# Optimization experiments

Measured on AMD Instinct MI355X. Metric: run time of the kernel, lower is better.

The kernel has to match this reference:

```python
import jax, jax.numpy as jnp
import numpy as np
import math

B, P = 64, 2048
E_DRUG, E_PATH = 512, 512
ATTN_DIM, H, DEPTH = 1024, 8, 1
HD = ATTN_DIM // (2 * H)          # head_dim = 64
SCALING = HD ** (-0.5)
LAMBDA_INIT = 0.8 - 0.6 * math.exp(-0.3 * DEPTH)
EPS_SM = 1e-20
EPS_RMS = 1e-5


def stable_softmax(x, eps=EPS_SM):
    x = x.astype(jnp.float32)
    x = x - jnp.max(x, axis=-1, keepdims=True)
    ex = jnp.exp(x)
    return ex / (jnp.sum(ex, axis=-1, keepdims=True) + eps)


def setup_inputs() -> dict:
    key = jax.random.key(0)
    ks = jax.random.split(key, 11)
    d = 2 * H * HD  # = ATTN_DIM
    return {
        "query": jax.random.normal(ks[0], (B, 1, E_DRUG), jnp.float32),
        "key": jax.random.normal(ks[1], (B, P, E_PATH), jnp.float32),
        # Linear weights stored [in, out] (transpose of torch storage; same math)
        "Wq": jax.random.normal(ks[2], (E_DRUG, d), jnp.float32) * 0.02,
        "Wk": jax.random.normal(ks[3], (E_PATH, d), jnp.float32) * 0.02,
        "Wv": jax.random.normal(ks[4], (E_PATH, d), jnp.float32) * 0.02,
        "Wo": jax.random.normal(ks[5], (d, E_DRUG), jnp.float32) * 0.02,
        "lambda_q1": jax.random.normal(ks[6], (HD,), jnp.float32) * 0.1,
        "lambda_k1": jax.random.normal(ks[7], (HD,), jnp.float32) * 0.1,
        "lambda_q2": jax.random.normal(ks[8], (HD,), jnp.float32) * 0.1,
        "lambda_k2": jax.random.normal(ks[9], (HD,), jnp.float32) * 0.1,
        "rms_weight": jnp.ones((2 * HD,), jnp.float32),
    }


def reference(query, key, Wq, Wk, Wv, Wo,
              lambda_q1, lambda_k1, lambda_q2, lambda_k2, rms_weight):
    # Q: [B,1,H,2,HD] -> [B,H,2,1,HD]; K,V: [B,P,H,2,HD] -> [B,H,2,P,HD]
    Q = (query @ Wq).reshape(B, 1, H, 2, HD).transpose(0, 2, 3, 1, 4) * SCALING
    K = (key @ Wk).reshape(B, P, H, 2, HD).transpose(0, 2, 3, 1, 4)
    V = (key @ Wv).reshape(B, P, H, 2, HD)

    # scores: [B,H,2,1,P]
    scores = jnp.einsum('bhsqd,bhskd->bhsqk', Q, K)
    scores = stable_softmax(scores)

    lam1 = jnp.exp(jnp.sum(lambda_q1 * lambda_k1))
    lam2 = jnp.exp(jnp.sum(lambda_q2 * lambda_k2))
    lam = lam1 - lam2 + LAMBDA_INIT

    diff_attn = scores[:, :, 0] - lam * scores[:, :, 1]  # [B,H,1,P]

    V_cat = V.transpose(0, 2, 1, 3, 4).reshape(B, H, P, 2 * HD)  # [B,H,P,2HD]
    out = jnp.einsum('bhqp,bhpd->bhqd', diff_attn, V_cat)        # [B,H,1,2HD]

    # RMSNorm over last dim, affine
    var = jnp.mean(out * out, axis=-1, keepdims=True)
    out = out * jax.lax.rsqrt(var + EPS_RMS) * rms_weight
    out = out * (1.0 - LAMBDA_INIT)

    out = out.transpose(0, 2, 1, 3).reshape(B, 1, 2 * H * HD)
    out = out @ Wo  # [B,1,E_DRUG]
    return out, diff_attn
```

## Files before the change

kernel.cpp:

```cpp
#include <hip/hip_runtime.h>
#include <hip/hip_bf16.h>
#include <math.h>

#define B_ 64
#define P_ 2048
#define E_ 512
#define H_ 8
#define HD_ 64
#define D_ 1024
#define NC_ 16
#define CP_ 128
#define SMEM_FUSED (131072 + 8512 + 4352)

static constexpr float SCALING_C = 0.125f;
static constexpr float LAMBDA_INIT_C = 0.35550906759096966f;

typedef float f32x4 __attribute__((ext_vector_type(4)));
typedef float f32x2 __attribute__((ext_vector_type(2)));
typedef short bf16x8 __attribute__((ext_vector_type(8)));
typedef short bf16x4 __attribute__((ext_vector_type(4)));

static __device__ __forceinline__ short f2bf(float f) {
    unsigned u = __builtin_bit_cast(unsigned, f);
    unsigned r = (u + 0x7fffu + ((u >> 16) & 1u)) >> 16;
    return (short)r;
}

__global__ __launch_bounds__(256) void k_qproj(const float* __restrict__ query,
                                               const float* __restrict__ Wq,
                                               const float* __restrict__ Wk,
                                               unsigned short* __restrict__ qkfrag) {
    int x = blockIdx.x, b = blockIdx.y, t = threadIdx.x;
    __shared__ float q[E_];
    __shared__ float qh[256];
    q[t] = query[b * E_ + t];
    q[t + 256] = query[b * E_ + t + 256];
    __syncthreads();
    {
        int j = x * 256 + t;
        const float* w = Wq + j;
        float s0 = 0.f, s1 = 0.f, s2 = 0.f, s3 = 0.f;
        #pragma unroll 4
        for (int e = 0; e < E_; e += 4) {
            s0 += q[e]     * w[(long)e * D_];
            s1 += q[e + 1] * w[(long)(e + 1) * D_];
            s2 += q[e + 2] * w[(long)(e + 2) * D_];
            s3 += q[e + 3] * w[(long)(e + 3) * D_];
        }
        qh[t] = ((s0 + s1) + (s2 + s3)) * SCALING_C;
    }
    __syncthreads();
    int hs_loc = t >> 6, l = t & 63;
    int hs = x * 4 + hs_loc;
    int e0 = l * 8;
    const float* qp = qh + hs_loc * 64;
    float acc[8];
    #pragma unroll
    for (int jj = 0; jj < 8; ++jj) {
        const f32x4* w = (const f32x4*)(Wk + (long)(e0 + jj) * D_ + hs * HD_);
        float s = 0.f;
        #pragma unroll
        for (int d4 = 0; d4 < 16; ++d4) {
            f32x4 wv = w[d4];
            s += qp[d4 * 4 + 0] * wv[0] + qp[d4 * 4 + 1] * wv[1]
               + qp[d4 * 4 + 2] * wv[2] + qp[d4 * 4 + 3] * wv[3];
        }
        acc[jj] = s;
    }
    bf16x8 v;
    #pragma unroll
    for (int jj = 0; jj < 8; ++jj) v[jj] = f2bf(acc[jj]);
    *(bf16x8*)(qkfrag + (((long)b * 16 + (l >> 2)) * 64 + (l & 3) * 16 + hs) * 8) = v;
}

__global__ __launch_bounds__(512, 2) void k_fused512(const float* __restrict__ key,
                                                     const unsigned short* __restrict__ qkfrag,
                                                     float* __restrict__ wexp,
                                                     float* __restrict__ ms, float* __restrict__ zs,
                                                     float* __restrict__ apart) {
    extern __shared__ __align__(16) char smem[];
    unsigned short* kswz = (unsigned short*)smem;
    float* scr           = (float*)(smem + 131072);
    unsigned short* wbf  = (unsigned short*)(smem + 131072 + 8512);

    int pc = blockIdx.x, b = blockIdx.y;
    int t = threadIdx.x, wv = t >> 6, l = t & 63;

    {
        int prow = wv * 16 + (l & 15);
        const float* kp = key + ((long)b * P_ + pc * CP_ + prow) * E_ + (l >> 4) * 8;
        const bf16x8* qf = (const bf16x8*)(qkfrag + (long)b * 16 * 64 * 8) + l;
        int ebase = (l >> 4) * 8;
        int xorv = ((prow & 7) << 3) ^ ((prow & 8) << 1);
        f32x4 acc = {0.f, 0.f, 0.f, 0.f};
        #pragma unroll
        for (int s = 0; s < 16; ++s) {
            f32x4 x0 = *(const f32x4*)(kp + s * 32);
            f32x4 x1 = *(const f32x4*)(kp + s * 32 + 4);
            bf16x8 a;
            a[0] = f2bf(x0[0]); a[1] = f2bf(x0[1]); a[2] = f2bf(x0[2]); a[3] = f2bf(x0[3]);
            a[4] = f2bf(x1[0]); a[5] = f2bf(x1[1]); a[6] = f2bf(x1[2]); a[7] = f2bf(x1[3]);
            *(bf16x8*)(kswz + prow * 512 + ((ebase + 32 * s) ^ xorv)) = a;
            bf16x8 bq = qf[s * 64];
            acc = __builtin_amdgcn_mfma_f32_16x16x32_bf16(a, bq, acc, 0, 0, 0);
        }
        #pragma unroll
        for (int r = 0; r < 4; ++r)
            scr[(l & 15) * 133 + wv * 16 + (l >> 4) * 4 + r] = acc[r];
    }
    __syncthreads();

    {
        int hs = t >> 5, i = t & 31;
        const float* sr = scr + hs * 133 + i * 4;
        float v0 = sr[0], v1 = sr[1], v2 = sr[2], v3 = sr[3];
        float m = fmaxf(fmaxf(v0, v1), fmaxf(v2, v3));
        #pragma unroll
        for (int o = 16; o > 0; o >>= 1) m = fmaxf(m, __shfl_xor(m, o));
        f32x4 ev;
        ev[0] = expf(v0 - m); ev[1] = expf(v1 - m); ev[2] = expf(v2 - m); ev[3] = expf(v3 - m);
        float z = ev[0] + ev[1] + ev[2] + ev[3];
        #pragma unroll
        for (int o = 16; o > 0; o >>= 1) z += __shfl_xor(z, o);
        *(f32x4*)(wexp + ((long)b * 16 + hs) * P_ + pc * CP_ + i * 4) = ev;
        bf16x4 wb;
        wb[0] = f2bf(ev[0]); wb[1] = f2bf(ev[1]); wb[2] = f2bf(ev[2]); wb[3] = f2bf(ev[3]);
        *(bf16x4*)(wbf + hs * 136 + i * 4) = wb;
        if (i == 0) {
            ms[((long)pc * B_ + b) * 16 + hs] = m;
            zs[((long)pc * B_ + b) * 16 + hs] = z;
        }
    }
    __syncthreads();

    {
        const unsigned short* wrow = wbf + (l & 15) * 136;
        long obase = ((long)pc * B_ + b) * 16 * E_;
        #pragma unroll
        for (int tile = 0; tile < 4; ++tile) {
            int e = wv * 64 + tile * 16 + (l & 15);
            f32x4 acc = {0.f, 0.f, 0.f, 0.f};
            #pragma unroll
            for (int ks = 0; ks < 4; ++ks) {
                int pbase = ks * 32 + (l >> 4) * 8;
                bf16x8 af = *(const bf16x8*)(wrow + pbase);
                bf16x8 bfv;
                int x2 = (pbase & 8) << 1;
                #pragma unroll
                for (int j = 0; j < 8; ++j) {
                    int p = pbase + j;
                    bfv[j] = (short)kswz[p * 512 + (e ^ (j << 3) ^ x2)];
                }
                acc = __builtin_amdgcn_mfma_f32_16x16x32_bf16(af, bfv, acc, 0, 0, 0);
            }
            #pragma unroll
            for (int r = 0; r < 4; ++r) {
                int hs = (l >> 4) * 4 + r;
                apart[obase + (long)hs * E_ + e] = acc[r];
            }
        }
    }
}

__global__ __launch_bounds__(256) void k_comb(const float* __restrict__ wexp,
                                              const float* __restrict__ ms, const float* __restrict__ zs,
                                              const float* __restrict__ apart,
                                              const float* __restrict__ lq1, const float* __restrict__ lk1,
                                              const float* __restrict__ lq2, const float* __restrict__ lk2,
                                              const float* __restrict__ Wv, const float* __restrict__ rmsw,
                                              float* __restrict__ out1, float* __restrict__ on) {
    int h = blockIdx.x, b = blockIdx.y, t = threadIdx.x;
    __shared__ float lam_s;
    __shared__ float mc0s[NC_], mc1s[NC_], zc0s[NC_], zc1s[NC_];
    __shared__ float c0s[NC_], c1s[NC_];
    __shared__ float attk[E_];
    __shared__ float onred[2][128];
    __shared__ float red[4];
    int hs0 = 2 * h, hs1 = 2 * h + 1;
    if (t < 64) {
        float v1 = lq1[t] * lk1[t];
        float v2 = lq2[t] * lk2[t];
        #pragma unroll
        for (int o = 32; o > 0; o >>= 1) { v1 += __shfl_xor(v1, o); v2 += __shfl_xor(v2, o); }
        if (t == 0) lam_s = expf(v1) - expf(v2) + LAMBDA_INIT_C;
    }
    if (t >= 64 && t < 64 + NC_) {
        int c = t - 64;
        mc0s[c] = ms[((long)c * B_ + b) * 16 + hs0];
        mc1s[c] = ms[((long)c * B_ + b) * 16 + hs1];
        zc0s[c] = zs[((long)c * B_ + b) * 16 + hs0];
        zc1s[c] = zs[((long)c * B_ + b) * 16 + hs1];
    }
    __syncthreads();
    float m0 = -3.0e38f, m1 = -3.0e38f;
    #pragma unroll
    for (int c = 0; c < NC_; ++c) { m0 = fmaxf(m0, mc0s[c]); m1 = fmaxf(m1, mc1s[c]); }
    float z0 = 0.f, z1 = 0.f;
    #pragma unroll
    for (int c = 0; c < NC_; ++c) {
        z0 += zc0s[c] * expf(mc0s[c] - m0);
        z1 += zc1s[c] * expf(mc1s[c] - m1);
    }
    float lam = lam_s;
    float i0 = 1.f / (z0 + 1e-20f);
    float i1 = lam / (z1 + 1e-20f);
    if (t < NC_) {
        c0s[t] = expf(mc0s[t] - m0) * i0;
        c1s[t] = expf(mc1s[t] - m1) * i1;
    }
    __syncthreads();
    const float* w0p = wexp + ((long)b * 16 + hs0) * P_;
    const float* w1p = wexp + ((long)b * 16 + hs1) * P_;
    float* dst = out1 + ((long)b * H_ + h) * P_;
    #pragma unroll
    for (int c8 = 0; c8 < 8; ++c8) {
        int p = c8 * 256 + t;
        dst[p] = w0p[p] * c0s[p >> 7] - w1p[p] * c1s[p >> 7];
    }
    #pragma unroll
    for (int k = 0; k < 2; ++k) {
        int e = k * 256 + t;
        float s = 0.f;
        #pragma unroll 8
        for (int c = 0; c < NC_; ++c) {
            s += c0s[c] * apart[(((long)c * B_ + b) * 16 + hs0) * E_ + e]
               - c1s[c] * apart[(((long)c * B_ + b) * 16 + hs1) * E_ + e];
        }
        attk[e] = s;
    }
    __syncthreads();
    int j = t & 127, half = t >> 7;
    const float* w = Wv + (long)(half * 256) * D_ + h * 128 + j;
    const float* aa = attk + half * 256;
    float s0 = 0.f, s1 = 0.f, s2 = 0.f, s3 = 0.f;
    #pragma unroll 8
    for (int e = 0; e < 256; e += 4) {
        s0 += aa[e]     * w[(long)e * D_];
        s1 += aa[e + 1] * w[(long)(e + 1) * D_];
        s2 += aa[e + 2] * w[(long)(e + 2) * D_];
        s3 += aa[e + 3] * w[(long)(e + 3) * D_];
    }
    onred[half][j] = (s0 + s1) + (s2 + s3);
    __syncthreads();
    float v = 0.f;
    if (t < 128) v = onred[0][t] + onred[1][t];
    float sq = v * v;
    int wv2 = t >> 6, ln = t & 63;
    #pragma unroll
    for (int o = 32; o > 0; o >>= 1) sq += __shfl_xor(sq, o);
    if (ln == 0) red[wv2] = sq;
    __syncthreads();
    float tot = red[0] + red[1];
    float scale = rsqrtf(tot * (1.f / 128.f) + 1e-5f) * (1.f - LAMBDA_INIT_C);
    if (t < 128) on[(long)b * D_ + h * 128 + t] = v * scale * rmsw[t];
}

__global__ __launch_bounds__(256) void k_wo(const float* __restrict__ on,
                                            const float* __restrict__ Wo,
                                            float* __restrict__ wop) {
    int kc = blockIdx.x >> 1, oc = blockIdx.x & 1, b = blockIdx.y;
    int t = threadIdx.x;
    __shared__ float sh[256];
    sh[t] = on[(long)b * D_ + kc * 256 + t];
    __syncthreads();
    int o = oc * 256 + t;
    const float* w = Wo + (long)(kc * 256) * 512 + o;
    float s0 = 0.f, s1 = 0.f, s2 = 0.f, s3 = 0.f;
    #pragma unroll 8
    for (int k = 0; k < 256; k += 4) {
        s0 += sh[k]     * w[(long)k * 512];
        s1 += sh[k + 1] * w[(long)(k + 1) * 512];
        s2 += sh[k + 2] * w[(long)(k + 2) * 512];
        s3 += sh[k + 3] * w[(long)(k + 3) * 512];
    }
    wop[((long)kc * B_ + b) * 512 + o] = (s0 + s1) + (s2 + s3);
}

__global__ __launch_bounds__(256) void k_wored(const float* __restrict__ wop,
                                               float* __restrict__ out0) {
    int b = blockIdx.x, t = threadIdx.x;
    #pragma unroll
    for (int i = 0; i < 2; ++i) {
        int o = i * 256 + t;
        float s = 0.f;
        #pragma unroll
        for (int kc = 0; kc < 4; ++kc) s += wop[((long)kc * B_ + b) * 512 + o];
        out0[(long)b * 512 + o] = s;
    }
}

extern "C" void kernel_launch(void* const* d_in, const int* in_sizes, int n_in,
                              void* d_out, int out_size, void* d_ws, size_t ws_size,
                              hipStream_t stream) {
    const float* query = (const float*)d_in[0];
    const float* key   = (const float*)d_in[1];
    const float* Wq    = (const float*)d_in[2];
    const float* Wk    = (const float*)d_in[3];
    const float* Wv    = (const float*)d_in[4];
    const float* Wo    = (const float*)d_in[5];
    const float* lq1   = (const float*)d_in[6];
    const float* lk1   = (const float*)d_in[7];
    const float* lq2   = (const float*)d_in[8];
    const float* lk2   = (const float*)d_in[9];
    const float* rmsw  = (const float*)d_in[10];

    float* out0 = (float*)d_out;
    float* out1 = out0 + B_ * E_;

    unsigned short* qkfrag = (unsigned short*)d_ws;
    float* wexp  = (float*)d_ws + 262144;
    float* apart = wexp + (long)B_ * 16 * P_;
    float* ms    = apart + (long)NC_ * B_ * 16 * E_;
    float* zs    = ms + NC_ * B_ * 16;
    float* on    = zs + NC_ * B_ * 16;
    float* wop   = on + B_ * D_;

    static int smem_set = 0;
    if (!smem_set) {
        hipFuncSetAttribute((const void*)k_fused512,
                            hipFuncAttributeMaxDynamicSharedMemorySize, SMEM_FUSED);
        smem_set = 1;
    }

    hipLaunchKernelGGL(k_qproj,    dim3(4, B_),   dim3(256), 0, stream, query, Wq, Wk, qkfrag);
    hipLaunchKernelGGL(k_fused512, dim3(NC_, B_), dim3(512), SMEM_FUSED, stream,
                       key, qkfrag, wexp, ms, zs, apart);
    hipLaunchKernelGGL(k_comb,     dim3(H_, B_),  dim3(256), 0, stream, wexp, ms, zs, apart,
                       lq1, lk1, lq2, lk2, Wv, rmsw, out1, on);
    hipLaunchKernelGGL(k_wo,       dim3(8, B_),   dim3(256), 0, stream, on, Wo, wop);
    hipLaunchKernelGGL(k_wored,    dim3(B_),      dim3(256), 0, stream, wop, out0);
}
```

Baseline: 141.1 us.

## Halve key chunk size, store partial attention outputs as bf16 in e-major layout

The fused kernel now processes 64-position chunks with 256 threads, doubling the grid to 32 chunks per batch and roughly halving LDS use per block, which lets more blocks fit on each CU. The per-chunk attention partials are written as bf16 in an [e][16] layout, so the combine kernel reads both heads of a pair with one 32-bit load. This cuts the partial-buffer traffic, but there are twice as many chunks to combine and the partials lose precision to bf16. The attribute call is now made on every launch.

```diff
diff --git a/kernel.cpp b/kernel.cpp
--- a/kernel.cpp
+++ b/kernel.cpp
@@ -8,9 +8,11 @@
 #define H_ 8
 #define HD_ 64
 #define D_ 1024
-#define NC_ 16
-#define CP_ 128
-#define SMEM_FUSED (131072 + 8512 + 4352)
+#define NC_ 32
+#define CP_ 64
+#define SCR_ 68
+#define WBF_ 72
+#define SMEM_FUSED (65536 + 4352 + 2304)
 
 static constexpr float SCALING_C = 0.125f;
 static constexpr float LAMBDA_INIT_C = 0.35550906759096966f;
@@ -24,6 +26,9 @@
     unsigned u = __builtin_bit_cast(unsigned, f);
     unsigned r = (u + 0x7fffu + ((u >> 16) & 1u)) >> 16;
     return (short)r;
+}
+static __device__ __forceinline__ float bf2f(unsigned short s) {
+    return __builtin_bit_cast(float, (unsigned)s << 16);
 }
 
 __global__ __launch_bounds__(256) void k_qproj(const float* __restrict__ query,
@@ -73,15 +78,15 @@
     *(bf16x8*)(qkfrag + (((long)b * 16 + (l >> 2)) * 64 + (l & 3) * 16 + hs) * 8) = v;
 }
 
-__global__ __launch_bounds__(512, 2) void k_fused512(const float* __restrict__ key,
+__global__ __launch_bounds__(256, 2) void k_fused256(const float* __restrict__ key,
                                                      const unsigned short* __restrict__ qkfrag,
                                                      float* __restrict__ wexp,
                                                      float* __restrict__ ms, float* __restrict__ zs,
-                                                     float* __restrict__ apart) {
+                                                     unsigned short* __restrict__ apart) {
     extern __shared__ __align__(16) char smem[];
     unsigned short* kswz = (unsigned short*)smem;
-    float* scr           = (float*)(smem + 131072);
-    unsigned short* wbf  = (unsigned short*)(smem + 131072 + 8512);
+    float* scr           = (float*)(smem + 65536);
+    unsigned short* wbf  = (unsigned short*)(smem + 65536 + 4352);
 
     int pc = blockIdx.x, b = blockIdx.y;
     int t = threadIdx.x, wv = t >> 6, l = t & 63;
@@ -106,26 +111,26 @@
         }
         #pragma unroll
         for (int r = 0; r < 4; ++r)
-            scr[(l & 15) * 133 + wv * 16 + (l >> 4) * 4 + r] = acc[r];
+            scr[(l & 15) * SCR_ + wv * 16 + (l >> 4) * 4 + r] = acc[r];
     }
     __syncthreads();
 
     {
-        int hs = t >> 5, i = t & 31;
-        const float* sr = scr + hs * 133 + i * 4;
+        int hs = t >> 4, i = t & 15;
+        const float* sr = scr + hs * SCR_ + i * 4;
         float v0 = sr[0], v1 = sr[1], v2 = sr[2], v3 = sr[3];
         float m = fmaxf(fmaxf(v0, v1), fmaxf(v2, v3));
         #pragma unroll
-        for (int o = 16; o > 0; o >>= 1) m = fmaxf(m, __shfl_xor(m, o));
+        for (int o = 8; o > 0; o >>= 1) m = fmaxf(m, __shfl_xor(m, o));
         f32x4 ev;
         ev[0] = expf(v0 - m); ev[1] = expf(v1 - m); ev[2] = expf(v2 - m); ev[3] = expf(v3 - m);
         float z = ev[0] + ev[1] + ev[2] + ev[3];
         #pragma unroll
-        for (int o = 16; o > 0; o >>= 1) z += __shfl_xor(z, o);
+        for (int o = 8; o > 0; o >>= 1) z += __shfl_xor(z, o);
         *(f32x4*)(wexp + ((long)b * 16 + hs) * P_ + pc * CP_ + i * 4) = ev;
         bf16x4 wb;
         wb[0] = f2bf(ev[0]); wb[1] = f2bf(ev[1]); wb[2] = f2bf(ev[2]); wb[3] = f2bf(ev[3]);
-        *(bf16x4*)(wbf + hs * 136 + i * 4) = wb;
+        *(bf16x4*)(wbf + hs * WBF_ + i * 4) = wb;
         if (i == 0) {
             ms[((long)pc * B_ + b) * 16 + hs] = m;
             zs[((long)pc * B_ + b) * 16 + hs] = z;
@@ -134,14 +139,14 @@
     __syncthreads();
 
     {
-        const unsigned short* wrow = wbf + (l & 15) * 136;
-        long obase = ((long)pc * B_ + b) * 16 * E_;
-        #pragma unroll
-        for (int tile = 0; tile < 4; ++tile) {
-            int e = wv * 64 + tile * 16 + (l & 15);
+        const unsigned short* wrow = wbf + (l & 15) * WBF_;
+        long obase = ((long)pc * B_ + b) * 512 * 16;
+        #pragma unroll
+        for (int tile = 0; tile < 8; ++tile) {
+            int e = wv * 128 + tile * 16 + (l & 15);
             f32x4 acc = {0.f, 0.f, 0.f, 0.f};
             #pragma unroll
-            for (int ks = 0; ks < 4; ++ks) {
+            for (int ks = 0; ks < 2; ++ks) {
                 int pbase = ks * 32 + (l >> 4) * 8;
                 bf16x8 af = *(const bf16x8*)(wrow + pbase);
                 bf16x8 bfv;
@@ -153,18 +158,16 @@
                 }
                 acc = __builtin_amdgcn_mfma_f32_16x16x32_bf16(af, bfv, acc, 0, 0, 0);
             }
-            #pragma unroll
-            for (int r = 0; r < 4; ++r) {
-                int hs = (l >> 4) * 4 + r;
-                apart[obase + (long)hs * E_ + e] = acc[r];
-            }
+            bf16x4 ob;
+            ob[0] = f2bf(acc[0]); ob[1] = f2bf(acc[1]); ob[2] = f2bf(acc[2]); ob[3] = f2bf(acc[3]);
+            *(bf16x4*)(apart + obase + (long)e * 16 + (l >> 4) * 4) = ob;
         }
     }
 }
 
 __global__ __launch_bounds__(256) void k_comb(const float* __restrict__ wexp,
                                               const float* __restrict__ ms, const float* __restrict__ zs,
-                                              const float* __restrict__ apart,
+                                              const unsigned short* __restrict__ apart,
                                               const float* __restrict__ lq1, const float* __restrict__ lk1,
                                               const float* __restrict__ lq2, const float* __restrict__ lk2,
                                               const float* __restrict__ Wv, const float* __restrict__ rmsw,
@@ -215,16 +218,18 @@
     #pragma unroll
     for (int c8 = 0; c8 < 8; ++c8) {
         int p = c8 * 256 + t;
-        dst[p] = w0p[p] * c0s[p >> 7] - w1p[p] * c1s[p >> 7];
+        dst[p] = w0p[p] * c0s[p >> 6] - w1p[p] * c1s[p >> 6];
     }
     #pragma unroll
     for (int k = 0; k < 2; ++k) {
         int e = k * 256 + t;
         float s = 0.f;
+        long base = (long)b * 512 * 16 + (long)e * 16 + hs0;
         #pragma unroll 8
         for (int c = 0; c < NC_; ++c) {
-            s += c0s[c] * apart[(((long)c * B_ + b) * 16 + hs0) * E_ + e]
-               - c1s[c] * apart[(((long)c * B_ + b) * 16 + hs1) * E_ + e];
+            unsigned pr = *(const unsigned*)(apart + base + (long)c * B_ * 512 * 16);
+            s += c0s[c] * bf2f((unsigned short)pr)
+               - c1s[c] * bf2f((unsigned short)(pr >> 16));
         }
         attk[e] = s;
     }
@@ -309,21 +314,17 @@
 
     unsigned short* qkfrag = (unsigned short*)d_ws;
     float* wexp  = (float*)d_ws + 262144;
-    float* apart = wexp + (long)B_ * 16 * P_;
-    float* ms    = apart + (long)NC_ * B_ * 16 * E_;
+    unsigned short* apart = (unsigned short*)(wexp + (long)B_ * 16 * P_);
+    float* ms    = wexp + (long)B_ * 16 * P_ + 8388608;
     float* zs    = ms + NC_ * B_ * 16;
     float* on    = zs + NC_ * B_ * 16;
     float* wop   = on + B_ * D_;
 
-    static int smem_set = 0;
-    if (!smem_set) {
-        hipFuncSetAttribute((const void*)k_fused512,
-                            hipFuncAttributeMaxDynamicSharedMemorySize, SMEM_FUSED);
-        smem_set = 1;
-    }
+    hipFuncSetAttribute((const void*)k_fused256,
+                        hipFuncAttributeMaxDynamicSharedMemorySize, SMEM_FUSED);
 
     hipLaunchKernelGGL(k_qproj,    dim3(4, B_),   dim3(256), 0, stream, query, Wq, Wk, qkfrag);
-    hipLaunchKernelGGL(k_fused512, dim3(NC_, B_), dim3(512), SMEM_FUSED, stream,
+    hipLaunchKernelGGL(k_fused256, dim3(NC_, B_), dim3(256), SMEM_FUSED, stream,
                        key, qkfrag, wexp, ms, zs, apart);
     hipLaunchKernelGGL(k_comb,     dim3(H_, B_),  dim3(256), 0, stream, wexp, ms, zs, apart,
                        lq1, lk1, lq2, lk2, Wv, rmsw, out1, on);
```

Measured after the change: 166.7 us. 1.18x slower.

## Loop fused kernel over 64-row sub-chunks with online softmax and register prefetch

Applied to the files above, without the earlier changes.

The fused score/attention kernel now processes 512 positions per block in eight 64-row sub-chunks. It keeps a running max per head and rescales its register accumulators, so the partial attention output written to global memory shrinks by a factor of four. The next sub-chunk of key is prefetched into registers while the current one is converted and multiplied, and LDS use is halved. The cost is more block-level barriers per block, a grid of only 256 blocks, and extra work in the combine kernel to rebuild per-group scale factors from the per-chunk maxima.

```diff
diff --git a/kernel.cpp b/kernel.cpp
--- a/kernel.cpp
+++ b/kernel.cpp
@@ -6,11 +6,10 @@
 #define P_ 2048
 #define E_ 512
 #define H_ 8
-#define HD_ 64
 #define D_ 1024
-#define NC_ 16
-#define CP_ 128
-#define SMEM_FUSED (131072 + 8512 + 4352)
+#define NC_ 32
+#define NG_ 4
+#define SMEM_FUSED (65536 + 8704 + 2304 + 64 + 64)
 
 static constexpr float SCALING_C = 0.125f;
 static constexpr float LAMBDA_INIT_C = 0.35550906759096966f;
@@ -18,7 +17,6 @@
 typedef float f32x4 __attribute__((ext_vector_type(4)));
 typedef float f32x2 __attribute__((ext_vector_type(2)));
 typedef short bf16x8 __attribute__((ext_vector_type(8)));
-typedef short bf16x4 __attribute__((ext_vector_type(4)));
 
 static __device__ __forceinline__ short f2bf(float f) {
     unsigned u = __builtin_bit_cast(unsigned, f);
@@ -57,7 +55,7 @@
     float acc[8];
     #pragma unroll
     for (int jj = 0; jj < 8; ++jj) {
-        const f32x4* w = (const f32x4*)(Wk + (long)(e0 + jj) * D_ + hs * HD_);
+        const f32x4* w = (const f32x4*)(Wk + (long)(e0 + jj) * D_ + hs * 64);
         float s = 0.f;
         #pragma unroll
         for (int d4 = 0; d4 < 16; ++d4) {
@@ -73,91 +71,138 @@
     *(bf16x8*)(qkfrag + (((long)b * 16 + (l >> 2)) * 64 + (l & 3) * 16 + hs) * 8) = v;
 }
 
-__global__ __launch_bounds__(512, 2) void k_fused512(const float* __restrict__ key,
-                                                     const unsigned short* __restrict__ qkfrag,
-                                                     float* __restrict__ wexp,
-                                                     float* __restrict__ ms, float* __restrict__ zs,
-                                                     float* __restrict__ apart) {
+__global__ __launch_bounds__(512, 2) void k_fusedp(const float* __restrict__ key,
+                                                   const unsigned short* __restrict__ qkfrag,
+                                                   float* __restrict__ wexp,
+                                                   float* __restrict__ ms, float* __restrict__ zs,
+                                                   float* __restrict__ apart) {
     extern __shared__ __align__(16) char smem[];
     unsigned short* kswz = (unsigned short*)smem;
-    float* scr           = (float*)(smem + 131072);
-    unsigned short* wbf  = (unsigned short*)(smem + 131072 + 8512);
-
-    int pc = blockIdx.x, b = blockIdx.y;
+    float* scr           = (float*)(smem + 65536);
+    unsigned short* wbf  = (unsigned short*)(smem + 74240);
+    float* fac_l         = (float*)(smem + 76544);
+    float* mrun_l        = (float*)(smem + 76608);
+
+    int pcg = blockIdx.x, b = blockIdx.y;
     int t = threadIdx.x, wv = t >> 6, l = t & 63;
-
+    int rt = wv >> 1, eh = wv & 1;
+    int prow = rt * 16 + (l & 15);
+    int xorv = ((prow & 7) << 3) ^ ((prow & 8) << 1);
+    int ebase = eh * 256 + (l >> 4) * 8;
+
+    if (t < 16) mrun_l[t] = -3.0e38f;
+
+    bf16x8 qfr[8];
     {
-        int prow = wv * 16 + (l & 15);
-        const float* kp = key + ((long)b * P_ + pc * CP_ + prow) * E_ + (l >> 4) * 8;
-        const bf16x8* qf = (const bf16x8*)(qkfrag + (long)b * 16 * 64 * 8) + l;
-        int ebase = (l >> 4) * 8;
-        int xorv = ((prow & 7) << 3) ^ ((prow & 8) << 1);
-        f32x4 acc = {0.f, 0.f, 0.f, 0.f};
-        #pragma unroll
-        for (int s = 0; s < 16; ++s) {
-            f32x4 x0 = *(const f32x4*)(kp + s * 32);
-            f32x4 x1 = *(const f32x4*)(kp + s * 32 + 4);
-            bf16x8 a;
-            a[0] = f2bf(x0[0]); a[1] = f2bf(x0[1]); a[2] = f2bf(x0[2]); a[3] = f2bf(x0[3]);
-            a[4] = f2bf(x1[0]); a[5] = f2bf(x1[1]); a[6] = f2bf(x1[2]); a[7] = f2bf(x1[3]);
-            *(bf16x8*)(kswz + prow * 512 + ((ebase + 32 * s) ^ xorv)) = a;
-            bf16x8 bq = qf[s * 64];
-            acc = __builtin_amdgcn_mfma_f32_16x16x32_bf16(a, bq, acc, 0, 0, 0);
-        }
-        #pragma unroll
-        for (int r = 0; r < 4; ++r)
-            scr[(l & 15) * 133 + wv * 16 + (l >> 4) * 4 + r] = acc[r];
-    }
-    __syncthreads();
+        const bf16x8* qf = (const bf16x8*)(qkfrag + (long)b * 16 * 64 * 8);
+        #pragma unroll
+        for (int s = 0; s < 8; ++s) qfr[s] = qf[(eh * 8 + s) * 64 + l];
+    }
+
+    const float* kp = key + ((long)b * P_ + pcg * 512 + prow) * E_ + ebase;
+
+    f32x4 x[16];
+    #pragma unroll
+    for (int s = 0; s < 8; ++s) {
+        x[2 * s]     = *(const f32x4*)(kp + s * 32);
+        x[2 * s + 1] = *(const f32x4*)(kp + s * 32 + 4);
+    }
+
+    f32x4 accp[4];
+    #pragma unroll
+    for (int i = 0; i < 4; ++i) accp[i] = {0.f, 0.f, 0.f, 0.f};
+
+    for (int c = 0; c < 8; ++c) {
+        {
+            f32x4 acc = {0.f, 0.f, 0.f, 0.f};
+            #pragma unroll
+            for (int s = 0; s < 8; ++s) {
+                f32x4 x0 = x[2 * s], x1 = x[2 * s + 1];
+                bf16x8 a;
+                a[0] = f2bf(x0[0]); a[1] = f2bf(x0[1]); a[2] = f2bf(x0[2]); a[3] = f2bf(x0[3]);
+                a[4] = f2bf(x1[0]); a[5] = f2bf(x1[1]); a[6] = f2bf(x1[2]); a[7] = f2bf(x1[3]);
+                *(bf16x8*)(kswz + prow * 512 + ((ebase + s * 32) ^ xorv)) = a;
+                acc = __builtin_amdgcn_mfma_f32_16x16x32_bf16(a, qfr[s], acc, 0, 0, 0);
+            }
+            #pragma unroll
+            for (int r = 0; r < 4; ++r)
+                scr[eh * 1088 + (l & 15) * 68 + rt * 16 + (l >> 4) * 4 + r] = acc[r];
+        }
+        if (c < 7) {
+            const float* kpn = kp + (long)(c + 1) * 64 * E_;
+            #pragma unroll
+            for (int s = 0; s < 8; ++s) {
+                x[2 * s]     = *(const f32x4*)(kpn + s * 32);
+                x[2 * s + 1] = *(const f32x4*)(kpn + s * 32 + 4);
+            }
+        }
+        __syncthreads();
+
+        {
+            int hs = t >> 5, i = t & 31;
+            const float* s0p = scr + hs * 68 + i * 2;
+            const float* s1p = s0p + 1088;
+            float v0 = s0p[0] + s1p[0];
+            float v1 = s0p[1] + s1p[1];
+            float m = fmaxf(v0, v1);
+            #pragma unroll
+            for (int o = 16; o > 0; o >>= 1) m = fmaxf(m, __shfl_xor(m, o));
+            float e0v = expf(v0 - m), e1v = expf(v1 - m);
+            float z = e0v + e1v;
+            #pragma unroll
+            for (int o = 16; o > 0; o >>= 1) z += __shfl_xor(z, o);
+            float mold = mrun_l[hs];
+            float mnew = fmaxf(mold, m);
+            float wsc = expf(m - mnew);
+            if (i == 0) {
+                mrun_l[hs] = mnew;
+                fac_l[hs] = expf(mold - mnew);
+                ms[((long)(pcg * 8 + c) * B_ + b) * 16 + hs] = m;
+                zs[((long)(pcg * 8 + c) * B_ + b) * 16 + hs] = z;
+            }
+            f32x2 wv2; wv2[0] = e0v; wv2[1] = e1v;
+            *(f32x2*)(wexp + ((long)b * 16 + hs) * P_ + pcg * 512 + c * 64 + i * 2) = wv2;
+            unsigned lo = (unsigned short)f2bf(e0v * wsc);
+            unsigned hi = (unsigned short)f2bf(e1v * wsc);
+            *(unsigned*)(wbf + hs * 72 + i * 2) = lo | (hi << 16);
+        }
+        __syncthreads();
+
+        {
+            f32x4 frv;
+            frv[0] = fac_l[(l >> 4) * 4 + 0];
+            frv[1] = fac_l[(l >> 4) * 4 + 1];
+            frv[2] = fac_l[(l >> 4) * 4 + 2];
+            frv[3] = fac_l[(l >> 4) * 4 + 3];
+            const unsigned short* wrow = wbf + (l & 15) * 72;
+            #pragma unroll
+            for (int tile = 0; tile < 4; ++tile) {
+                accp[tile] = accp[tile] * frv;
+                int e = wv * 64 + tile * 16 + (l & 15);
+                #pragma unroll
+                for (int ks = 0; ks < 2; ++ks) {
+                    int pbase = ks * 32 + (l >> 4) * 8;
+                    bf16x8 af = *(const bf16x8*)(wrow + pbase);
+                    int x2 = (pbase & 8) << 1;
+                    bf16x8 bfv;
+                    #pragma unroll
+                    for (int j = 0; j < 8; ++j)
+                        bfv[j] = (short)kswz[(pbase + j) * 512 + (e ^ (j << 3) ^ x2)];
+                    accp[tile] = __builtin_amdgcn_mfma_f32_16x16x32_bf16(af, bfv, accp[tile], 0, 0, 0);
+                }
+            }
+        }
+        __syncthreads();
+    }
 
     {
-        int hs = t >> 5, i = t & 31;
-        const float* sr = scr + hs * 133 + i * 4;
-        float v0 = sr[0], v1 = sr[1], v2 = sr[2], v3 = sr[3];
-        float m = fmaxf(fmaxf(v0, v1), fmaxf(v2, v3));
-        #pragma unroll
-        for (int o = 16; o > 0; o >>= 1) m = fmaxf(m, __shfl_xor(m, o));
-        f32x4 ev;
-        ev[0] = expf(v0 - m); ev[1] = expf(v1 - m); ev[2] = expf(v2 - m); ev[3] = expf(v3 - m);
-        float z = ev[0] + ev[1] + ev[2] + ev[3];
-        #pragma unroll
-        for (int o = 16; o > 0; o >>= 1) z += __shfl_xor(z, o);
-        *(f32x4*)(wexp + ((long)b * 16 + hs) * P_ + pc * CP_ + i * 4) = ev;
-        bf16x4 wb;
-        wb[0] = f2bf(ev[0]); wb[1] = f2bf(ev[1]); wb[2] = f2bf(ev[2]); wb[3] = f2bf(ev[3]);
-        *(bf16x4*)(wbf + hs * 136 + i * 4) = wb;
-        if (i == 0) {
-            ms[((long)pc * B_ + b) * 16 + hs] = m;
-            zs[((long)pc * B_ + b) * 16 + hs] = z;
-        }
-    }
-    __syncthreads();
-
-    {
-        const unsigned short* wrow = wbf + (l & 15) * 136;
-        long obase = ((long)pc * B_ + b) * 16 * E_;
+        long abase = ((long)pcg * B_ + b) * 16 * E_;
         #pragma unroll
         for (int tile = 0; tile < 4; ++tile) {
             int e = wv * 64 + tile * 16 + (l & 15);
-            f32x4 acc = {0.f, 0.f, 0.f, 0.f};
-            #pragma unroll
-            for (int ks = 0; ks < 4; ++ks) {
-                int pbase = ks * 32 + (l >> 4) * 8;
-                bf16x8 af = *(const bf16x8*)(wrow + pbase);
-                bf16x8 bfv;
-                int x2 = (pbase & 8) << 1;
-                #pragma unroll
-                for (int j = 0; j < 8; ++j) {
-                    int p = pbase + j;
-                    bfv[j] = (short)kswz[p * 512 + (e ^ (j << 3) ^ x2)];
-                }
-                acc = __builtin_amdgcn_mfma_f32_16x16x32_bf16(af, bfv, acc, 0, 0, 0);
-            }
-            #pragma unroll
-            for (int r = 0; r < 4; ++r) {
-                int hs = (l >> 4) * 4 + r;
-                apart[obase + (long)hs * E_ + e] = acc[r];
-            }
+            #pragma unroll
+            for (int r = 0; r < 4; ++r)
+                apart[abase + (long)((l >> 4) * 4 + r) * E_ + e] = accp[tile][r];
         }
     }
 }
@@ -215,16 +260,28 @@
     #pragma unroll
     for (int c8 = 0; c8 < 8; ++c8) {
         int p = c8 * 256 + t;
-        dst[p] = w0p[p] * c0s[p >> 7] - w1p[p] * c1s[p >> 7];
+        dst[p] = w0p[p] * c0s[p >> 6] - w1p[p] * c1s[p >> 6];
+    }
+    float cg0[NG_], cg1[NG_];
+    #pragma unroll
+    for (int g = 0; g < NG_; ++g) {
+        float mg0 = -3.0e38f, mg1 = -3.0e38f;
+        #pragma unroll
+        for (int q = 0; q < 8; ++q) {
+            mg0 = fmaxf(mg0, mc0s[g * 8 + q]);
+            mg1 = fmaxf(mg1, mc1s[g * 8 + q]);
+        }
+        cg0[g] = expf(mg0 - m0) * i0;
+        cg1[g] = expf(mg1 - m1) * i1;
     }
     #pragma unroll
     for (int k = 0; k < 2; ++k) {
         int e = k * 256 + t;
         float s = 0.f;
-        #pragma unroll 8
-        for (int c = 0; c < NC_; ++c) {
-            s += c0s[c] * apart[(((long)c * B_ + b) * 16 + hs0) * E_ + e]
-               - c1s[c] * apart[(((long)c * B_ + b) * 16 + hs1) * E_ + e];
+        #pragma unroll
+        for (int g = 0; g < NG_; ++g) {
+            s += cg0[g] * apart[(((long)g * B_ + b) * 16 + hs0) * E_ + e]
+               - cg1[g] * apart[(((long)g * B_ + b) * 16 + hs1) * E_ + e];
         }
         attk[e] = s;
     }
@@ -310,23 +367,19 @@
     unsigned short* qkfrag = (unsigned short*)d_ws;
     float* wexp  = (float*)d_ws + 262144;
     float* apart = wexp + (long)B_ * 16 * P_;
-    float* ms    = apart + (long)NC_ * B_ * 16 * E_;
+    float* ms    = apart + (long)NG_ * B_ * 16 * E_;
     float* zs    = ms + NC_ * B_ * 16;
     float* on    = zs + NC_ * B_ * 16;
     float* wop   = on + B_ * D_;
 
-    static int smem_set = 0;
-    if (!smem_set) {
-        hipFuncSetAttribute((const void*)k_fused512,
-                            hipFuncAttributeMaxDynamicSharedMemorySize, SMEM_FUSED);
-        smem_set = 1;
-    }
-
-    hipLaunchKernelGGL(k_qproj,    dim3(4, B_),   dim3(256), 0, stream, query, Wq, Wk, qkfrag);
-    hipLaunchKernelGGL(k_fused512, dim3(NC_, B_), dim3(512), SMEM_FUSED, stream,
+    hipFuncSetAttribute((const void*)k_fusedp,
+                        hipFuncAttributeMaxDynamicSharedMemorySize, SMEM_FUSED);
+
+    hipLaunchKernelGGL(k_qproj,  dim3(4, B_),   dim3(256), 0, stream, query, Wq, Wk, qkfrag);
+    hipLaunchKernelGGL(k_fusedp, dim3(NG_, B_), dim3(512), SMEM_FUSED, stream,
                        key, qkfrag, wexp, ms, zs, apart);
-    hipLaunchKernelGGL(k_comb,     dim3(H_, B_),  dim3(256), 0, stream, wexp, ms, zs, apart,
+    hipLaunchKernelGGL(k_comb,   dim3(H_, B_),  dim3(256), 0, stream, wexp, ms, zs, apart,
                        lq1, lk1, lq2, lk2, Wv, rmsw, out1, on);
-    hipLaunchKernelGGL(k_wo,       dim3(8, B_),   dim3(256), 0, stream, on, Wo, wop);
-    hipLaunchKernelGGL(k_wored,    dim3(B_),      dim3(256), 0, stream, wop, out0);
-}
+    hipLaunchKernelGGL(k_wo,     dim3(8, B_),   dim3(256), 0, stream, on, Wo, wop);
+    hipLaunchKernelGGL(k_wored,  dim3(B_),      dim3(256), 0, stream, wop, out0);
+}
```

After: 123.7 us. 12.3% less time.
